# Optimization experiments

Measured on AMD Instinct MI355X. Metric: run time of the kernel, lower is better.

## Reference

```python
import math
import jax, jax.numpy as jnp
import numpy as np

EMBED_DIM = 512
NUM_HEADS = 8
PROJ_DIM = EMBED_DIM // NUM_HEADS
ATTN_WINDOW = 5
HALF_WINDOW = (ATTN_WINDOW - 1) // 2  # 2
ATTN_PARAM = 1.0
ATTN_DISPLACEMENT = 1
# per-head positions: ['center','left','right','center'] repeated to 8 heads (synst repeats short lists)
HEAD_SHIFTS = np.array([0, -ATTN_DISPLACEMENT, ATTN_DISPLACEMENT, 0] * 2, dtype=np.int32)


def _xavier(key, shape):
    fan_in, fan_out = shape[1], shape[0]
    bound = math.sqrt(6.0 / (fan_in + fan_out))
    return jax.random.uniform(key, shape, jnp.float32, -bound, bound)


def setup_inputs() -> dict:
    key = jax.random.key(0)
    k1, k2, k3, k4, k5 = jax.random.split(key, 5)
    B, S, E = 8, 4096, EMBED_DIM
    return {
        "values": jax.random.normal(k1, (B, S, E), jnp.float32),
        "keys": jax.random.normal(k2, (B, S, E), jnp.float32),
        "queries": jax.random.normal(k3, (B, S, E), jnp.float32),
        "input_weights": _xavier(k4, (E, E)),        # value projection (attn_weights=1, non-learned type)
        "out_proj_w": _xavier(k5, (E, E)),           # output_projection.weight (bias=False)
    }


def reference(values, keys, queries, input_weights, out_proj_w):
    # keys/queries are unused by the hard-coded 'normal' attention path (no QK^T)
    B, S, E = values.shape
    H, Dh, hw, W = NUM_HEADS, PROJ_DIM, HALF_WINDOW, ATTN_WINDOW

    # value projection + head split: [B,S,E] -> [B,H,S,Dh]
    v = values @ input_weights.T
    v = v.reshape(B, S, H, Dh).transpose(0, 2, 1, 3)

    # fixed Gaussian filter over relative distances [-hw, hw] (unnormalized pdf, as in the source)
    dist = jnp.arange(-hw, hw + 1, dtype=jnp.float32)
    filt = (1.0 / (ATTN_PARAM * math.sqrt(2.0 * math.pi))) * jnp.exp(-0.5 * (dist / ATTN_PARAM) ** 2)  # [W]

    shifts = jnp.asarray(HEAD_SHIFTS)            # [H] per-head center displacement
    P = hw + int(np.max(np.abs(HEAD_SHIFTS)))    # pad so all gathers are in range
    vp = jnp.pad(v, ((0, 0), (0, 0), (P, P), (0, 0)))  # [B,H,S+2P,Dh]

    h_ar = jnp.arange(H)[:, None]                # [H,1]
    pos = jnp.arange(S)[None, :]                 # [1,S]
    out = jnp.zeros_like(v)
    for j in range(W):                           # tiny fixed window loop (W=5)
        idx = pos + P + shifts[:, None] + (j - hw)   # [H,S]
        out = out + filt[j] * vp[:, h_ar, idx, :]    # [B,H,S,Dh]

    out = out.transpose(0, 2, 1, 3).reshape(B, S, E)
    return out @ out_proj_w.T
```

## Files before the change

kernel.cpp:

```cpp
#include <hip/hip_runtime.h>
#include <hip/hip_bf16.h>
#include <stdint.h>

typedef __bf16 bf16;
typedef __bf16 bf16x8 __attribute__((ext_vector_type(8)));
typedef float  f32x4  __attribute__((ext_vector_type(4)));

#define BM 128
#define BN 64
#define BK 64
#define E  512
#define SB 4112
#define M1 (8 * SB)
#define M2 32768

__device__ __forceinline__ void gl_lds_16(const bf16* g, bf16* l) {
    __builtin_amdgcn_global_load_lds(
        (__attribute__((address_space(1))) void*)g,
        (__attribute__((address_space(3))) void*)l,
        16, 0, 0);
}


__global__ __launch_bounds__(256)
void gemm_bt_bf16(const bf16* __restrict__ A, const bf16* __restrict__ Bm,
                  bf16* __restrict__ C, int M, int N, int K)
{
    __shared__ bf16 As[BM * BK];
    __shared__ bf16 Bs[BN * BK];

    const int tid  = threadIdx.x;
    const int nq   = gridDim.x >> 3;
    const int orig = (blockIdx.x & 7) * nq + (blockIdx.x >> 3);
    const int bm   = orig >> 3;
    const int bn   = orig & 7;
    const int wave = tid >> 6;
    const int lane = tid & 63;
    const int wm   = wave >> 1;
    const int wn   = wave & 1;

    const int srow = tid >> 3;
    const int scol = (((tid & 7) ^ (srow & 7)) << 3);
    const size_t a_off = (size_t)(bm * BM + srow) * K + scol;
    const size_t b_off = (size_t)(bn * BN + srow) * K + scol;
    const int    l_off = tid * 8;

    f32x4 acc[4][2] = {};
    const int fr = lane & 15;
    const int q  = lane >> 4;

    for (int k0 = 0; k0 < K; k0 += BK) {
#pragma unroll
        for (int c = 0; c < 4; ++c)
            gl_lds_16(A + a_off + (size_t)(c * 32) * K + k0, As + c * 2048 + l_off);
#pragma unroll
        for (int c = 0; c < 2; ++c)
            gl_lds_16(Bm + b_off + (size_t)(c * 32) * K + k0, Bs + c * 2048 + l_off);
        __syncthreads();

#pragma unroll
        for (int t = 0; t < 2; ++t) {
            bf16x8 af[4], bfr[2];
#pragma unroll
            for (int i = 0; i < 4; ++i) {
                const int Ra = wm * 64 + i * 16 + fr;
                const int c  = t * 4 + q;
                af[i] = *(const bf16x8*)(As + Ra * BK + ((c ^ (Ra & 7)) << 3));
            }
#pragma unroll
            for (int j = 0; j < 2; ++j) {
                const int Rb = wn * 32 + j * 16 + fr;
                const int c  = t * 4 + q;
                bfr[j] = *(const bf16x8*)(Bs + Rb * BK + ((c ^ (Rb & 7)) << 3));
            }
#pragma unroll
            for (int i = 0; i < 4; ++i)
#pragma unroll
                for (int j = 0; j < 2; ++j)
                    acc[i][j] = __builtin_amdgcn_mfma_f32_16x16x32_bf16(af[i], bfr[j], acc[i][j], 0, 0, 0);
        }
        __syncthreads();
    }

    const int crow = (lane >> 4) << 2;
    const int ccol = lane & 15;
    const int row0 = bm * BM + wm * 64 + crow;
    const int col0 = bn * BN + wn * 32 + ccol;
#pragma unroll
    for (int i = 0; i < 4; ++i)
#pragma unroll
        for (int j = 0; j < 2; ++j)
#pragma unroll
            for (int r = 0; r < 4; ++r)
                C[(size_t)(row0 + i * 16 + r) * N + (col0 + j * 16)] = (bf16)acc[i][j][r];
}

__global__ __launch_bounds__(256)
void gemm2_gather(const bf16* __restrict__ P, const bf16* __restrict__ Bm,
                  float* __restrict__ C)
{
    __shared__ bf16 As[BM * BK];
    __shared__ bf16 Bs[BN * BK];

    const int tid  = threadIdx.x;
    const int nq   = gridDim.x >> 3;
    const int orig = (blockIdx.x & 7) * nq + (blockIdx.x >> 3);
    const int bm   = orig >> 3;
    const int bn   = orig & 7;
    const int wave = tid >> 6;
    const int lane = tid & 63;
    const int wm   = wave >> 1;
    const int wn   = wave & 1;

    const int srow = tid >> 3;
    const int scol = (((tid & 7) ^ (srow & 7)) << 3);
    const size_t b_off = (size_t)(bn * BN + srow) * E + scol;
    const int    l_off = tid * 8;

    f32x4 acc[4][2] = {};
    const int fr = lane & 15;
    const int q  = lane >> 4;

    for (int k0 = 0; k0 < E; k0 += BK) {
        const int h3 = (k0 >> 6) & 3;
        const int sh = (h3 == 1) ? -1 : (h3 == 2) ? 1 : 0;
#pragma unroll
        for (int c = 0; c < 4; ++c) {
            const int m = bm * BM + c * 32 + srow;
            const int prow = (m >> 12) * SB + (m & 4095) + 1 + sh;
            gl_lds_16(P + (size_t)prow * E + k0 + scol, As + c * 2048 + l_off);
        }
#pragma unroll
        for (int c = 0; c < 2; ++c)
            gl_lds_16(Bm + b_off + (size_t)(c * 32) * E + k0, Bs + c * 2048 + l_off);
        __syncthreads();

#pragma unroll
        for (int t = 0; t < 2; ++t) {
            bf16x8 af[4], bfr[2];
#pragma unroll
            for (int i = 0; i < 4; ++i) {
                const int Ra = wm * 64 + i * 16 + fr;
                const int c  = t * 4 + q;
                af[i] = *(const bf16x8*)(As + Ra * BK + ((c ^ (Ra & 7)) << 3));
            }
#pragma unroll
            for (int j = 0; j < 2; ++j) {
                const int Rb = wn * 32 + j * 16 + fr;
                const int c  = t * 4 + q;
                bfr[j] = *(const bf16x8*)(Bs + Rb * BK + ((c ^ (Rb & 7)) << 3));
            }
#pragma unroll
            for (int i = 0; i < 4; ++i)
#pragma unroll
                for (int j = 0; j < 2; ++j)
                    acc[i][j] = __builtin_amdgcn_mfma_f32_16x16x32_bf16(af[i], bfr[j], acc[i][j], 0, 0, 0);
        }
        __syncthreads();
    }

    const int crow = (lane >> 4) << 2;
    const int ccol = lane & 15;
    const int row0 = bm * BM + wm * 64 + crow;
    const int col0 = bn * BN + wn * 32 + ccol;
#pragma unroll
    for (int i = 0; i < 4; ++i)
#pragma unroll
        for (int j = 0; j < 2; ++j)
#pragma unroll
            for (int r = 0; r < 4; ++r)
                C[(size_t)(row0 + i * 16 + r) * E + (col0 + j * 16)] = acc[i][j][r];
}

__global__ __launch_bounds__(256)
void prep(const float* __restrict__ vals, const float* __restrict__ w_in,
          const float* __restrict__ w_out, bf16* __restrict__ vg,
          bf16* __restrict__ win_b, bf16* __restrict__ wout_b)
{
    const int tid = threadIdx.x;
    const int blk = blockIdx.x;

    if (blk < 256) {
        const int i = blk * 256 + tid;
        const int half = (E * E) / 8;
        const float* src = (i < half) ? w_in : w_out;
        bf16* dst        = (i < half) ? win_b : wout_b;
        const int k = (i < half) ? i : i - half;
        const f32x4* p = (const f32x4*)src + 2 * (size_t)k;
        f32x4 a = p[0], bq = p[1];
        bf16x8 o;
        o[0] = (bf16)a[0];  o[1] = (bf16)a[1];  o[2] = (bf16)a[2];  o[3] = (bf16)a[3];
        o[4] = (bf16)bq[0]; o[5] = (bf16)bq[1]; o[6] = (bf16)bq[2]; o[7] = (bf16)bq[3];
        *((bf16x8*)dst + k) = o;
        return;
    }

    const int e8   = tid & 63;
    const int gidx = (blk - 256) * 4 + (tid >> 6);
    const int m0   = gidx << 3;
    const int b    = m0 / SB;
    const int r0   = m0 - b * SB;

    const float filt[5] = {0.05399096651318806f, 0.24197072451914337f,
                           0.3989422804014327f,
                           0.24197072451914337f, 0.05399096651318806f};

    float acc[8][8];
#pragma unroll
    for (int t = 0; t < 8; ++t)
#pragma unroll
        for (int d = 0; d < 8; ++d) acc[t][d] = 0.f;

    const float* bbase = vals + (size_t)b * 4096 * E + e8 * 8;
#pragma unroll
    for (int u = 0; u < 12; ++u) {
        const int sp = r0 - 3 + u;
        if (sp >= 0 && sp < 4096) {
            const f32x4* p = (const f32x4*)(bbase + (size_t)sp * E);
            const f32x4 x0 = p[0], x1 = p[1];
            const float x[8] = {x0[0], x0[1], x0[2], x0[3],
                                x1[0], x1[1], x1[2], x1[3]};
#pragma unroll
            for (int t = 0; t < 8; ++t) {
                const int j = u - t;
                if (j >= 0 && j < 5) {
                    const float w = filt[j];
#pragma unroll
                    for (int d = 0; d < 8; ++d) acc[t][d] += w * x[d];
                }
            }
        }
    }
#pragma unroll
    for (int t = 0; t < 8; ++t) {
        bf16x8 o;
#pragma unroll
        for (int d = 0; d < 8; ++d) o[d] = (bf16)acc[t][d];
        *((bf16x8*)vg + (size_t)(m0 + t) * 64 + e8) = o;
    }
}

extern "C" void kernel_launch(void* const* d_in, const int* in_sizes, int n_in,
                              void* d_out, int out_size, void* d_ws, size_t ws_size,
                              hipStream_t stream)
{
    const float* values = (const float*)d_in[0];
    const float* w_in   = (const float*)d_in[3];
    const float* w_out  = (const float*)d_in[4];
    float* out = (float*)d_out;

    bf16* win_b  = (bf16*)d_ws;
    bf16* wout_b = win_b + E * E;
    bf16* vg     = wout_b + E * E;
    bf16* Pbuf   = vg + (size_t)M1 * E;

    prep<<<256 + M1 / 32, 256, 0, stream>>>(values, w_in, w_out, vg, win_b, wout_b);

    gemm_bt_bf16<<<(M1 / BM) * 8, 256, 0, stream>>>(vg, win_b, Pbuf, M1, E, E);
    gemm2_gather<<<(M2 / BM) * 8, 256, 0, stream>>>(Pbuf, wout_b, out);
}
```

Baseline: 236.4 us.

## Fuse windowed Gaussian smoothing into first GEMM A-tile loading

Removes the separate prep pass that wrote a smoothed bf16 copy of the values; the first GEMM now computes the 5-tap filter directly from fp32 values while filling its A tile in LDS. Weight conversion moves to its own small kernel. This avoids writing and re-reading the intermediate, but each of the 8 N-column blocks recomputes the same A tile from fp32 with 5 overlapping row reads, and the loads become synchronous register loads instead of async global-to-LDS copies.

```diff
diff --git a/kernel.cpp b/kernel.cpp
--- a/kernel.cpp
+++ b/kernel.cpp
@@ -22,9 +22,9 @@
 }
 
 
-__global__ __launch_bounds__(256)
-void gemm_bt_bf16(const bf16* __restrict__ A, const bf16* __restrict__ Bm,
-                  bf16* __restrict__ C, int M, int N, int K)
+__global__ __launch_bounds__(256, 4)
+void gemm1_fused(const float* __restrict__ vals, const bf16* __restrict__ Bm,
+                 bf16* __restrict__ C)
 {
     __shared__ bf16 As[BM * BK];
     __shared__ bf16 Bs[BN * BK];
@@ -41,21 +41,56 @@
 
     const int srow = tid >> 3;
     const int scol = (((tid & 7) ^ (srow & 7)) << 3);
-    const size_t a_off = (size_t)(bm * BM + srow) * K + scol;
-    const size_t b_off = (size_t)(bn * BN + srow) * K + scol;
+    const size_t b_off = (size_t)(bn * BN + srow) * E + scol;
     const int    l_off = tid * 8;
+
+    const int ach = tid & 7;
+    const int arg = tid >> 3;
+    int  sbase[4];
+    const float* vb[4];
+#pragma unroll
+    for (int u = 0; u < 4; ++u) {
+        const int m = bm * BM + arg * 4 + u;
+        const int b = m / SB;
+        sbase[u] = (m - b * SB) - 3;
+        vb[u] = vals + (size_t)b * 4096 * E + ach * 8;
+    }
+
+    const float filt[5] = {0.05399096651318806f, 0.24197072451914337f,
+                           0.3989422804014327f,
+                           0.24197072451914337f, 0.05399096651318806f};
 
     f32x4 acc[4][2] = {};
     const int fr = lane & 15;
     const int q  = lane >> 4;
 
-    for (int k0 = 0; k0 < K; k0 += BK) {
-#pragma unroll
-        for (int c = 0; c < 4; ++c)
-            gl_lds_16(A + a_off + (size_t)(c * 32) * K + k0, As + c * 2048 + l_off);
+    for (int k0 = 0; k0 < E; k0 += BK) {
 #pragma unroll
         for (int c = 0; c < 2; ++c)
-            gl_lds_16(Bm + b_off + (size_t)(c * 32) * K + k0, Bs + c * 2048 + l_off);
+            gl_lds_16(Bm + b_off + (size_t)(c * 32) * E + k0, Bs + c * 2048 + l_off);
+
+#pragma unroll
+        for (int u = 0; u < 4; ++u) {
+            float a8[8] = {0.f, 0.f, 0.f, 0.f, 0.f, 0.f, 0.f, 0.f};
+#pragma unroll
+            for (int j = 0; j < 5; ++j) {
+                const int sp = sbase[u] + j;
+                if (sp >= 0 && sp < 4096) {
+                    const f32x4* p = (const f32x4*)(vb[u] + (size_t)sp * E + k0);
+                    const f32x4 x0 = p[0], x1 = p[1];
+                    const float w = filt[j];
+                    a8[0] += w * x0[0]; a8[1] += w * x0[1];
+                    a8[2] += w * x0[2]; a8[3] += w * x0[3];
+                    a8[4] += w * x1[0]; a8[5] += w * x1[1];
+                    a8[6] += w * x1[2]; a8[7] += w * x1[3];
+                }
+            }
+            bf16x8 o;
+#pragma unroll
+            for (int d = 0; d < 8; ++d) o[d] = (bf16)a8[d];
+            const int r = arg * 4 + u;
+            *(bf16x8*)(As + r * BK + ((ach ^ (r & 7)) << 3)) = o;
+        }
         __syncthreads();
 
 #pragma unroll
@@ -92,7 +127,7 @@
         for (int j = 0; j < 2; ++j)
 #pragma unroll
             for (int r = 0; r < 4; ++r)
-                C[(size_t)(row0 + i * 16 + r) * N + (col0 + j * 16)] = (bf16)acc[i][j][r];
+                C[(size_t)(row0 + i * 16 + r) * E + (col0 + j * 16)] = (bf16)acc[i][j][r];
 }
 
 __global__ __launch_bounds__(256)
@@ -173,71 +208,20 @@
 }
 
 __global__ __launch_bounds__(256)
-void prep(const float* __restrict__ vals, const float* __restrict__ w_in,
-          const float* __restrict__ w_out, bf16* __restrict__ vg,
-          bf16* __restrict__ win_b, bf16* __restrict__ wout_b)
-{
-    const int tid = threadIdx.x;
-    const int blk = blockIdx.x;
-
-    if (blk < 256) {
-        const int i = blk * 256 + tid;
-        const int half = (E * E) / 8;
-        const float* src = (i < half) ? w_in : w_out;
-        bf16* dst        = (i < half) ? win_b : wout_b;
-        const int k = (i < half) ? i : i - half;
-        const f32x4* p = (const f32x4*)src + 2 * (size_t)k;
-        f32x4 a = p[0], bq = p[1];
-        bf16x8 o;
-        o[0] = (bf16)a[0];  o[1] = (bf16)a[1];  o[2] = (bf16)a[2];  o[3] = (bf16)a[3];
-        o[4] = (bf16)bq[0]; o[5] = (bf16)bq[1]; o[6] = (bf16)bq[2]; o[7] = (bf16)bq[3];
-        *((bf16x8*)dst + k) = o;
-        return;
-    }
-
-    const int e8   = tid & 63;
-    const int gidx = (blk - 256) * 4 + (tid >> 6);
-    const int m0   = gidx << 3;
-    const int b    = m0 / SB;
-    const int r0   = m0 - b * SB;
-
-    const float filt[5] = {0.05399096651318806f, 0.24197072451914337f,
-                           0.3989422804014327f,
-                           0.24197072451914337f, 0.05399096651318806f};
-
-    float acc[8][8];
-#pragma unroll
-    for (int t = 0; t < 8; ++t)
-#pragma unroll
-        for (int d = 0; d < 8; ++d) acc[t][d] = 0.f;
-
-    const float* bbase = vals + (size_t)b * 4096 * E + e8 * 8;
-#pragma unroll
-    for (int u = 0; u < 12; ++u) {
-        const int sp = r0 - 3 + u;
-        if (sp >= 0 && sp < 4096) {
-            const f32x4* p = (const f32x4*)(bbase + (size_t)sp * E);
-            const f32x4 x0 = p[0], x1 = p[1];
-            const float x[8] = {x0[0], x0[1], x0[2], x0[3],
-                                x1[0], x1[1], x1[2], x1[3]};
-#pragma unroll
-            for (int t = 0; t < 8; ++t) {
-                const int j = u - t;
-                if (j >= 0 && j < 5) {
-                    const float w = filt[j];
-#pragma unroll
-                    for (int d = 0; d < 8; ++d) acc[t][d] += w * x[d];
-                }
-            }
-        }
-    }
-#pragma unroll
-    for (int t = 0; t < 8; ++t) {
-        bf16x8 o;
-#pragma unroll
-        for (int d = 0; d < 8; ++d) o[d] = (bf16)acc[t][d];
-        *((bf16x8*)vg + (size_t)(m0 + t) * 64 + e8) = o;
-    }
+void cvt_weights(const float* __restrict__ w_in, const float* __restrict__ w_out,
+                 bf16* __restrict__ win_b, bf16* __restrict__ wout_b)
+{
+    const int i = blockIdx.x * 256 + threadIdx.x;
+    const int half = (E * E) / 8;
+    const float* src = (i < half) ? w_in : w_out;
+    bf16* dst        = (i < half) ? win_b : wout_b;
+    const int k = (i < half) ? i : i - half;
+    const f32x4* p = (const f32x4*)src + 2 * (size_t)k;
+    f32x4 a = p[0], bq = p[1];
+    bf16x8 o;
+    o[0] = (bf16)a[0];  o[1] = (bf16)a[1];  o[2] = (bf16)a[2];  o[3] = (bf16)a[3];
+    o[4] = (bf16)bq[0]; o[5] = (bf16)bq[1]; o[6] = (bf16)bq[2]; o[7] = (bf16)bq[3];
+    *((bf16x8*)dst + k) = o;
 }
 
 extern "C" void kernel_launch(void* const* d_in, const int* in_sizes, int n_in,
@@ -251,11 +235,10 @@
 
     bf16* win_b  = (bf16*)d_ws;
     bf16* wout_b = win_b + E * E;
-    bf16* vg     = wout_b + E * E;
-    bf16* Pbuf   = vg + (size_t)M1 * E;
-
-    prep<<<256 + M1 / 32, 256, 0, stream>>>(values, w_in, w_out, vg, win_b, wout_b);
-
-    gemm_bt_bf16<<<(M1 / BM) * 8, 256, 0, stream>>>(vg, win_b, Pbuf, M1, E, E);
+    bf16* Pbuf   = wout_b + E * E;
+
+    cvt_weights<<<(2 * E * E / 8) / 256, 256, 0, stream>>>(w_in, w_out, win_b, wout_b);
+
+    gemm1_fused<<<(M1 / BM) * 8, 256, 0, stream>>>(values, win_b, Pbuf);
     gemm2_gather<<<(M2 / BM) * 8, 256, 0, stream>>>(Pbuf, wout_b, out);
 }
```

Measured after the change: 341.8 us. +44.6%, slower.
